# Optimization experiments

Hardware: AMD Instinct MI355X
Metric: run time of the kernel (lower is better)

The kernel has to match this reference:

```python
import jax, jax.numpy as jnp
import numpy as np
import math

HEADS = 16
ROPE_BASE = 10000.0


def _alibi_slopes(n):
    # power-of-2 branch of ALiBiBias._get_slopes (n=16 is a power of 2)
    start = 2.0 ** (-(2.0 ** (-(math.log2(n) - 3))))
    return np.array([start * (start ** i) for i in range(n)], dtype=np.float32)


def _rope_cos_sin(T, head_dim):
    # RotaryPositionalEmbedding: inv_freq over even indices, emb = cat(freqs, freqs)
    inv_freq = 1.0 / (ROPE_BASE ** (jnp.arange(0, head_dim, 2, dtype=jnp.float32) / head_dim))
    t = jnp.arange(T, dtype=jnp.float32)
    f = t[:, None] * inv_freq[None, :]            # (T, head_dim//2)
    emb = jnp.concatenate([f, f], axis=-1)        # (T, head_dim)
    # apply_rotary_pos_emb takes cos/sin of emb then strides [0::2]
    cos = jnp.cos(emb)[:, 0::2]                   # (T, head_dim//2)
    sin = jnp.sin(emb)[:, 0::2]
    return cos, sin


def _apply_rope(x, cos, sin):
    # x: (B,H,T,hd); cos/sin: (T, hd//2)
    x1 = x[..., 0::2]
    x2 = x[..., 1::2]
    r1 = x1 * cos - x2 * sin
    r2 = x2 * cos + x1 * sin
    # interleave back: out[...,0::2]=r1, out[...,1::2]=r2
    return jnp.stack([r1, r2], axis=-1).reshape(x.shape)


def setup_inputs() -> dict:
    key = jax.random.key(0)
    k1, k2, k3, k4 = jax.random.split(key, 4)
    B, T, C = 2, 2048, 1024
    x = jax.random.normal(k1, (B, T, C), dtype=jnp.float32)
    W_qkv = jax.random.normal(k2, (C, 3 * C), dtype=jnp.float32) * 0.02
    W_out = jax.random.normal(k3, (C, C), dtype=jnp.float32) * 0.02
    b_out = jax.random.normal(k4, (C,), dtype=jnp.float32) * 0.02
    return {"x": x, "W_qkv": W_qkv, "W_out": W_out, "b_out": b_out}


def reference(x, W_qkv, W_out, b_out):
    B, T, C = x.shape
    H = HEADS
    hd = C // H

    qkv = (x @ W_qkv).reshape(B, T, 3, H, hd)
    qkv = jnp.transpose(qkv, (2, 0, 3, 1, 4))     # (3, B, H, T, hd)
    q, k, v = qkv[0], qkv[1], qkv[2]

    cos, sin = _rope_cos_sin(T, hd)
    q = _apply_rope(q, cos, sin)
    k = _apply_rope(k, cos, sin)

    scores = jnp.einsum('bhqd,bhkd->bhqk', q, k) / jnp.sqrt(jnp.float32(hd))

    # ALiBi bias: -slope_h * |i - j|
    slopes = jnp.asarray(_alibi_slopes(H))        # (H,)
    pos = jnp.arange(T, dtype=jnp.float32)
    dist = jnp.abs(pos[None, :] - pos[:, None])   # (T, T)
    scores = scores - slopes[None, :, None, None] * dist[None, None, :, :]

    attn = jax.nn.softmax(scores, axis=-1)
    out = jnp.einsum('bhqk,bhkd->bhqd', attn, v)  # (B,H,T,hd)
    out = jnp.transpose(out, (0, 2, 1, 3)).reshape(B, T, C)
    out = out @ W_out + b_out
    return out, attn
```

## Files before the change

### kernel.cpp

```cpp
#include <hip/hip_runtime.h>
#include <hip/hip_bf16.h>

typedef __bf16 bf16_t;
typedef __bf16 bf16x8 __attribute__((ext_vector_type(8)));
typedef float floatx4 __attribute__((ext_vector_type(4)));

#define NB 2
#define NT 2048
#define NC 1024
#define NH 16
#define HD 64
#define BT (NB*NT)

__global__ void k_cvt_x(const float* __restrict__ x, bf16_t* __restrict__ xb, int n){
  int i = (blockIdx.x*blockDim.x + threadIdx.x)*4;
  if (i >= n) return;
  float4 v = *(const float4*)(x+i);
  bf16_t o[4] = {(bf16_t)v.x,(bf16_t)v.y,(bf16_t)v.z,(bf16_t)v.w};
  *(uint2*)(xb+i) = *(const uint2*)o;
}

__global__ void k_cvt_t(const float* __restrict__ in, bf16_t* __restrict__ out, int K, int N){
  __shared__ float tile[32][33];
  int tid = threadIdx.x;
  int kt = blockIdx.y*32, nt = blockIdx.x*32;
  int row = tid>>3, c4 = (tid&7)*4;
  float4 v = *(const float4*)(in + (size_t)(kt+row)*N + nt + c4);
  tile[row][c4+0]=v.x; tile[row][c4+1]=v.y; tile[row][c4+2]=v.z; tile[row][c4+3]=v.w;
  __syncthreads();
  bf16_t o[4];
  #pragma unroll
  for (int i=0;i<4;i++) o[i] = (bf16_t)tile[c4+i][row];
  *(uint2*)(out + (size_t)(nt+row)*K + kt + c4) = *(const uint2*)o;
}

template<bool BIAS, bool OUTBF>
__global__ __launch_bounds__(256) void k_gemm(
    const bf16_t* __restrict__ A, const bf16_t* __restrict__ Bt,
    void* __restrict__ Cv, const float* __restrict__ bias, int M, int N, int K){
  __shared__ __align__(16) bf16_t As[64][32];
  __shared__ __align__(16) bf16_t Bs[128][32];
  int tid = threadIdx.x;
  int wave = tid>>6, lane = tid&63, quad = lane>>4, l15 = lane&15;
  int m0 = blockIdx.y*64, n0 = blockIdx.x*128;
  int wm = (wave>>1)*32, wn = (wave&1)*64;
  floatx4 acc[2][4];
  #pragma unroll
  for(int i=0;i<2;i++)
    #pragma unroll
    for(int j=0;j<4;j++) acc[i][j] = (floatx4){0.f,0.f,0.f,0.f};
  int arow = tid>>2, ac8 = (tid&3)*8;
  const bf16_t* Ag  = A  + (size_t)(m0+arow)*K + ac8;
  const bf16_t* Bg0 = Bt + (size_t)(n0+arow)*K + ac8;
  const bf16_t* Bg1 = Bt + (size_t)(n0+arow+64)*K + ac8;
  for (int k0=0;k0<K;k0+=32){
    *(bf16x8*)&As[arow][ac8]    = *(const bf16x8*)(Ag  + k0);
    *(bf16x8*)&Bs[arow][ac8]    = *(const bf16x8*)(Bg0 + k0);
    *(bf16x8*)&Bs[arow+64][ac8] = *(const bf16x8*)(Bg1 + k0);
    __syncthreads();
    bf16x8 af[2], bfr[4];
    #pragma unroll
    for(int mi=0;mi<2;mi++) af[mi]  = *(const bf16x8*)&As[wm+mi*16+l15][quad*8];
    #pragma unroll
    for(int ni=0;ni<4;ni++) bfr[ni] = *(const bf16x8*)&Bs[wn+ni*16+l15][quad*8];
    #pragma unroll
    for(int mi=0;mi<2;mi++)
      #pragma unroll
      for(int ni=0;ni<4;ni++)
        acc[mi][ni] = __builtin_amdgcn_mfma_f32_16x16x32_bf16(af[mi], bfr[ni], acc[mi][ni],0,0,0);
    __syncthreads();
  }
  #pragma unroll
  for(int ni=0;ni<4;ni++){
    int col = n0 + wn + ni*16 + l15;
    float bv = 0.f; if (BIAS) bv = bias[col];
    #pragma unroll
    for(int mi=0;mi<2;mi++){
      int rowb = m0 + wm + mi*16 + quad*4;
      #pragma unroll
      for(int r=0;r<4;r++){
        float v = acc[mi][ni][r] + bv;
        if (OUTBF) ((bf16_t*)Cv)[(size_t)(rowb+r)*N + col] = (bf16_t)v;
        else       ((float*)Cv)[(size_t)(rowb+r)*N + col]  = v;
      }
    }
  }
}

__global__ void k_rope(const bf16_t* __restrict__ qkv, bf16_t* __restrict__ Qb,
                       bf16_t* __restrict__ Kb, bf16_t* __restrict__ Vb){
  int p = blockIdx.x*blockDim.x + threadIdx.x;
  int r = p / 1536;
  int c = (p - r*1536)*2;
  int s = c >> 10, rem = c & 1023;
  int h = rem >> 6, d = rem & 63, j = d >> 1;
  int b = r >> 11, t = r & 2047;
  float x1 = (float)qkv[(size_t)r*3072 + c];
  float x2 = (float)qkv[(size_t)r*3072 + c + 1];
  float o1, o2;
  if (s < 2){
    float freq = exp2f(-0.8304820237218406f * (float)(j & 15));
    float ang = (float)t * freq;
    float sn, cs;
    sincosf(ang, &sn, &cs);
    o1 = x1*cs - x2*sn;
    o2 = x2*cs + x1*sn;
  } else { o1 = x1; o2 = x2; }
  bf16_t* dst = (s==0) ? Qb : (s==1 ? Kb : Vb);
  bf16_t o[2] = {(bf16_t)o1, (bf16_t)o2};
  *(unsigned int*)(dst + (size_t)((b*NH + h)*NT + t)*HD + d) = *(const unsigned int*)o;
}

__global__ __launch_bounds__(256) void k_attn(
    const bf16_t* __restrict__ Qb, const bf16_t* __restrict__ Kb, const bf16_t* __restrict__ Vb,
    float* __restrict__ attn, bf16_t* __restrict__ Ob){
  __shared__ __align__(16) bf16_t Ks[32][72];
  __shared__ __align__(16) bf16_t Vt[64][40];
  __shared__ __align__(16) bf16_t Ps[4][16][40];
  int tid = threadIdx.x;
  int wave = tid>>6, lane = tid&63, quad = lane>>4, l15 = lane&15;
  int qt = blockIdx.x, bh = blockIdx.y;
  int h = bh & (NH-1);
  float slope = exp2f(-0.5f*(float)(h+1));
  int qbase = qt*64 + wave*16;
  const bf16_t* qrow = Qb + ((size_t)bh*NT + qbase + l15)*HD;
  bf16x8 qa0 = *(const bf16x8*)(qrow + quad*8);
  bf16x8 qa1 = *(const bf16x8*)(qrow + 32 + quad*8);
  int sr = tid>>3, sc8 = (tid&7)*8;
  const bf16_t* kbase = Kb + ((size_t)bh*NT + sr)*HD + sc8;
  const bf16_t* vbase = Vb + ((size_t)bh*NT + sr)*HD + sc8;
  const floatx4 z4 = {0.f,0.f,0.f,0.f};

  float lsum[4] = {0.f,0.f,0.f,0.f};
  for (int k0=0;k0<NT;k0+=32){
    *(bf16x8*)&Ks[sr][sc8] = *(const bf16x8*)(kbase + (size_t)k0*HD);
    __syncthreads();
    #pragma unroll
    for (int nt=0;nt<2;nt++){
      bf16x8 kb0 = *(const bf16x8*)&Ks[nt*16+l15][quad*8];
      bf16x8 kb1 = *(const bf16x8*)&Ks[nt*16+l15][32+quad*8];
      floatx4 sv = __builtin_amdgcn_mfma_f32_16x16x32_bf16(qa0, kb0, z4,0,0,0);
      sv = __builtin_amdgcn_mfma_f32_16x16x32_bf16(qa1, kb1, sv,0,0,0);
      int kpos = k0 + nt*16 + l15;
      #pragma unroll
      for (int r=0;r<4;r++){
        int qpos = qbase + quad*4 + r;
        float sc = sv[r]*0.125f - slope*fabsf((float)(qpos - kpos));
        lsum[r] += __expf(sc);
      }
    }
    __syncthreads();
  }
  #pragma unroll
  for (int r=0;r<4;r++){
    #pragma unroll
    for (int off=1;off<16;off<<=1) lsum[r] += __shfl_xor(lsum[r], off, 16);
  }
  float invl[4];
  #pragma unroll
  for (int r=0;r<4;r++) invl[r] = 1.f / lsum[r];

  floatx4 oacc[4] = {z4,z4,z4,z4};
  float* attnrow = attn + (size_t)bh*NT*NT;
  for (int k0=0;k0<NT;k0+=32){
    *(bf16x8*)&Ks[sr][sc8] = *(const bf16x8*)(kbase + (size_t)k0*HD);
    bf16x8 vl = *(const bf16x8*)(vbase + (size_t)k0*HD);
    #pragma unroll
    for (int i=0;i<8;i++) Vt[sc8+i][sr] = vl[i];
    __syncthreads();
    #pragma unroll
    for (int nt=0;nt<2;nt++){
      bf16x8 kb0 = *(const bf16x8*)&Ks[nt*16+l15][quad*8];
      bf16x8 kb1 = *(const bf16x8*)&Ks[nt*16+l15][32+quad*8];
      floatx4 sv = __builtin_amdgcn_mfma_f32_16x16x32_bf16(qa0, kb0, z4,0,0,0);
      sv = __builtin_amdgcn_mfma_f32_16x16x32_bf16(qa1, kb1, sv,0,0,0);
      int kpos = k0 + nt*16 + l15;
      #pragma unroll
      for (int r=0;r<4;r++){
        int qpos = qbase + quad*4 + r;
        float sc = sv[r]*0.125f - slope*fabsf((float)(qpos - kpos));
        float pv = __expf(sc) * invl[r];
        attnrow[(size_t)qpos*NT + kpos] = pv;
        Ps[wave][quad*4+r][nt*16+l15] = (bf16_t)pv;
      }
    }
    __syncthreads();
    bf16x8 pa = *(const bf16x8*)&Ps[wave][l15][quad*8];
    #pragma unroll
    for (int dt=0;dt<4;dt++){
      bf16x8 vb = *(const bf16x8*)&Vt[dt*16+l15][quad*8];
      oacc[dt] = __builtin_amdgcn_mfma_f32_16x16x32_bf16(pa, vb, oacc[dt],0,0,0);
    }
    __syncthreads();
  }
  int b = bh >> 4;
  #pragma unroll
  for (int dt=0;dt<4;dt++){
    #pragma unroll
    for (int r=0;r<4;r++){
      int t = qbase + quad*4 + r;
      Ob[(size_t)(b*NT + t)*NC + h*HD + dt*16 + l15] = (bf16_t)oacc[dt][r];
    }
  }
}

extern "C" void kernel_launch(void* const* d_in, const int* in_sizes, int n_in,
                              void* d_out, int out_size, void* d_ws, size_t ws_size,
                              hipStream_t stream){
  const float* x    = (const float*)d_in[0];
  const float* Wqkv = (const float*)d_in[1];
  const float* Wout = (const float*)d_in[2];
  const float* bout = (const float*)d_in[3];
  (void)in_sizes; (void)n_in; (void)out_size; (void)ws_size;

  char* ws = (char*)d_ws;
  size_t off = 0;
  auto alloc = [&](size_t elems)->bf16_t* {
    bf16_t* p = (bf16_t*)(ws + off);
    off += ((elems*sizeof(bf16_t) + 255)/256)*256;
    return p;
  };
  bf16_t* Xb   = alloc((size_t)BT*NC);
  bf16_t* Wqt  = alloc((size_t)3*NC*NC);
  bf16_t* Wot  = alloc((size_t)NC*NC);
  bf16_t* QKVb = alloc((size_t)BT*3*NC);
  bf16_t* Qb   = alloc((size_t)NB*NH*NT*HD);
  bf16_t* Kb   = alloc((size_t)NB*NH*NT*HD);
  bf16_t* Vb   = alloc((size_t)NB*NH*NT*HD);
  bf16_t* Ob   = alloc((size_t)BT*NC);

  k_cvt_x<<<(BT*NC/4)/256, 256, 0, stream>>>(x, Xb, BT*NC);
  k_cvt_t<<<dim3(3*NC/32, NC/32), 256, 0, stream>>>(Wqkv, Wqt, NC, 3*NC);
  k_cvt_t<<<dim3(NC/32,   NC/32), 256, 0, stream>>>(Wout, Wot, NC, NC);
  k_gemm<false,true><<<dim3(3*NC/128, BT/64), 256, 0, stream>>>(Xb, Wqt, (void*)QKVb, nullptr, BT, 3*NC, NC);
  k_rope<<<(BT*1536)/256, 256, 0, stream>>>(QKVb, Qb, Kb, Vb);
  float* attn = (float*)d_out + (size_t)BT*NC;
  k_attn<<<dim3(NT/64, NB*NH), 256, 0, stream>>>(Qb, Kb, Vb, attn, Ob);
  k_gemm<true,false><<<dim3(NC/128, BT/64), 256, 0, stream>>>(Ob, Wot, d_out, bout, BT, NC, NC);
}
```

Measured before the change: 812.0 us.

## Use LDS direct loads in GEMM, pre-transpose V, drop LDS staging in attention

```diff
diff --git a/kernel.cpp b/kernel.cpp
--- a/kernel.cpp
+++ b/kernel.cpp
@@ -11,6 +11,13 @@
 #define NH 16
 #define HD 64
 #define BT (NB*NT)
+
+#define ASCALE 0.1803368801111204f
+
+__device__ __forceinline__ void gload16(const bf16_t* g, bf16_t* l){
+  __builtin_amdgcn_global_load_lds((const __attribute__((address_space(1))) void*)g,
+                                   (__attribute__((address_space(3))) void*)l, 16, 0, 0);
+}
 
 __global__ void k_cvt_x(const float* __restrict__ x, bf16_t* __restrict__ xb, int n){
   int i = (blockIdx.x*blockDim.x + threadIdx.x)*4;
@@ -38,33 +45,39 @@
 __global__ __launch_bounds__(256) void k_gemm(
     const bf16_t* __restrict__ A, const bf16_t* __restrict__ Bt,
     void* __restrict__ Cv, const float* __restrict__ bias, int M, int N, int K){
-  __shared__ __align__(16) bf16_t As[64][32];
-  __shared__ __align__(16) bf16_t Bs[128][32];
+  __shared__ __align__(16) bf16_t As[128*32];
+  __shared__ __align__(16) bf16_t Bs[128*32];
   int tid = threadIdx.x;
   int wave = tid>>6, lane = tid&63, quad = lane>>4, l15 = lane&15;
-  int m0 = blockIdx.y*64, n0 = blockIdx.x*128;
-  int wm = (wave>>1)*32, wn = (wave&1)*64;
-  floatx4 acc[2][4];
-  #pragma unroll
-  for(int i=0;i<2;i++)
+  int m0 = blockIdx.y*128, n0 = blockIdx.x*128;
+  int wm = (wave>>1)*64, wn = (wave&1)*64;
+  floatx4 acc[4][4];
+  #pragma unroll
+  for(int i=0;i<4;i++)
     #pragma unroll
     for(int j=0;j<4;j++) acc[i][j] = (floatx4){0.f,0.f,0.f,0.f};
-  int arow = tid>>2, ac8 = (tid&3)*8;
-  const bf16_t* Ag  = A  + (size_t)(m0+arow)*K + ac8;
-  const bf16_t* Bg0 = Bt + (size_t)(n0+arow)*K + ac8;
-  const bf16_t* Bg1 = Bt + (size_t)(n0+arow+64)*K + ac8;
+  int r0 = tid>>2, ch8 = (tid&3)*8;
+  const bf16_t* Ag0 = A  + (size_t)(m0+r0)*K    + ch8;
+  const bf16_t* Ag1 = A  + (size_t)(m0+r0+64)*K + ch8;
+  const bf16_t* Bg0 = Bt + (size_t)(n0+r0)*K    + ch8;
+  const bf16_t* Bg1 = Bt + (size_t)(n0+r0+64)*K + ch8;
+  bf16_t* Al0 = As + (size_t)tid*8;
+  bf16_t* Al1 = As + (size_t)(256+tid)*8;
+  bf16_t* Bl0 = Bs + (size_t)tid*8;
+  bf16_t* Bl1 = Bs + (size_t)(256+tid)*8;
   for (int k0=0;k0<K;k0+=32){
-    *(bf16x8*)&As[arow][ac8]    = *(const bf16x8*)(Ag  + k0);
-    *(bf16x8*)&Bs[arow][ac8]    = *(const bf16x8*)(Bg0 + k0);
-    *(bf16x8*)&Bs[arow+64][ac8] = *(const bf16x8*)(Bg1 + k0);
+    gload16(Ag0+k0, Al0);
+    gload16(Ag1+k0, Al1);
+    gload16(Bg0+k0, Bl0);
+    gload16(Bg1+k0, Bl1);
     __syncthreads();
-    bf16x8 af[2], bfr[4];
-    #pragma unroll
-    for(int mi=0;mi<2;mi++) af[mi]  = *(const bf16x8*)&As[wm+mi*16+l15][quad*8];
-    #pragma unroll
-    for(int ni=0;ni<4;ni++) bfr[ni] = *(const bf16x8*)&Bs[wn+ni*16+l15][quad*8];
-    #pragma unroll
-    for(int mi=0;mi<2;mi++)
+    bf16x8 af[4], bfr[4];
+    #pragma unroll
+    for(int mi=0;mi<4;mi++) af[mi]  = *(const bf16x8*)&As[(wm+mi*16+l15)*32 + quad*8];
+    #pragma unroll
+    for(int ni=0;ni<4;ni++) bfr[ni] = *(const bf16x8*)&Bs[(wn+ni*16+l15)*32 + quad*8];
+    #pragma unroll
+    for(int mi=0;mi<4;mi++)
       #pragma unroll
       for(int ni=0;ni<4;ni++)
         acc[mi][ni] = __builtin_amdgcn_mfma_f32_16x16x32_bf16(af[mi], bfr[ni], acc[mi][ni],0,0,0);
@@ -75,7 +88,7 @@
     int col = n0 + wn + ni*16 + l15;
     float bv = 0.f; if (BIAS) bv = bias[col];
     #pragma unroll
-    for(int mi=0;mi<2;mi++){
+    for(int mi=0;mi<4;mi++){
       int rowb = m0 + wm + mi*16 + quad*4;
       #pragma unroll
       for(int r=0;r<4;r++){
@@ -88,7 +101,7 @@
 }
 
 __global__ void k_rope(const bf16_t* __restrict__ qkv, bf16_t* __restrict__ Qb,
-                       bf16_t* __restrict__ Kb, bf16_t* __restrict__ Vb){
+                       bf16_t* __restrict__ Kb, bf16_t* __restrict__ VT){
   int p = blockIdx.x*blockDim.x + threadIdx.x;
   int r = p / 1536;
   int c = (p - r*1536)*2;
@@ -97,101 +110,91 @@
   int b = r >> 11, t = r & 2047;
   float x1 = (float)qkv[(size_t)r*3072 + c];
   float x2 = (float)qkv[(size_t)r*3072 + c + 1];
-  float o1, o2;
   if (s < 2){
     float freq = exp2f(-0.8304820237218406f * (float)(j & 15));
     float ang = (float)t * freq;
     float sn, cs;
     sincosf(ang, &sn, &cs);
-    o1 = x1*cs - x2*sn;
-    o2 = x2*cs + x1*sn;
-  } else { o1 = x1; o2 = x2; }
-  bf16_t* dst = (s==0) ? Qb : (s==1 ? Kb : Vb);
-  bf16_t o[2] = {(bf16_t)o1, (bf16_t)o2};
-  *(unsigned int*)(dst + (size_t)((b*NH + h)*NT + t)*HD + d) = *(const unsigned int*)o;
+    float o1 = x1*cs - x2*sn;
+    float o2 = x2*cs + x1*sn;
+    if (s == 0){ o1 *= ASCALE; o2 *= ASCALE; }
+    bf16_t* dst = (s==0) ? Qb : Kb;
+    bf16_t o[2] = {(bf16_t)o1, (bf16_t)o2};
+    *(unsigned int*)(dst + (size_t)((b*NH + h)*NT + t)*HD + d) = *(const unsigned int*)o;
+  } else {
+    size_t base = ((size_t)(b*NH + h)*HD + d)*NT + t;
+    VT[base]      = (bf16_t)x1;
+    VT[base + NT] = (bf16_t)x2;
+  }
 }
 
 __global__ __launch_bounds__(256) void k_attn(
-    const bf16_t* __restrict__ Qb, const bf16_t* __restrict__ Kb, const bf16_t* __restrict__ Vb,
+    const bf16_t* __restrict__ Qb, const bf16_t* __restrict__ Kb, const bf16_t* __restrict__ VT,
     float* __restrict__ attn, bf16_t* __restrict__ Ob){
-  __shared__ __align__(16) bf16_t Ks[32][72];
-  __shared__ __align__(16) bf16_t Vt[64][40];
   __shared__ __align__(16) bf16_t Ps[4][16][40];
   int tid = threadIdx.x;
   int wave = tid>>6, lane = tid&63, quad = lane>>4, l15 = lane&15;
-  int qt = blockIdx.x, bh = blockIdx.y;
+  int bh = blockIdx.x, qt = blockIdx.y;
   int h = bh & (NH-1);
-  float slope = exp2f(-0.5f*(float)(h+1));
+  float slopeL = 1.44269504f * exp2f(-0.5f*(float)(h+1));
   int qbase = qt*64 + wave*16;
   const bf16_t* qrow = Qb + ((size_t)bh*NT + qbase + l15)*HD;
   bf16x8 qa0 = *(const bf16x8*)(qrow + quad*8);
   bf16x8 qa1 = *(const bf16x8*)(qrow + 32 + quad*8);
-  int sr = tid>>3, sc8 = (tid&7)*8;
-  const bf16_t* kbase = Kb + ((size_t)bh*NT + sr)*HD + sc8;
-  const bf16_t* vbase = Vb + ((size_t)bh*NT + sr)*HD + sc8;
+  const bf16_t* kb_base = Kb + ((size_t)bh*NT + l15)*HD + quad*8;
+  const bf16_t* vt_base = VT + ((size_t)bh*HD + l15)*NT + quad*8;
   const floatx4 z4 = {0.f,0.f,0.f,0.f};
+  float qf[4];
+  #pragma unroll
+  for (int r=0;r<4;r++) qf[r] = (float)(qbase + quad*4 + r);
 
   float lsum[4] = {0.f,0.f,0.f,0.f};
+  #pragma unroll 4
+  for (int k16=0;k16<NT;k16+=16){
+    bf16x8 kb0 = *(const bf16x8*)(kb_base + (size_t)k16*HD);
+    bf16x8 kb1 = *(const bf16x8*)(kb_base + (size_t)k16*HD + 32);
+    floatx4 sv = __builtin_amdgcn_mfma_f32_16x16x32_bf16(qa0, kb0, z4,0,0,0);
+    sv = __builtin_amdgcn_mfma_f32_16x16x32_bf16(qa1, kb1, sv,0,0,0);
+    float kf = (float)(k16 + l15);
+    #pragma unroll
+    for (int r=0;r<4;r++)
+      lsum[r] += exp2f(__builtin_fmaf(-slopeL, fabsf(qf[r]-kf), sv[r]));
+  }
+  #pragma unroll
+  for (int r=0;r<4;r++){
+    #pragma unroll
+    for (int off=1;off<16;off<<=1) lsum[r] += __shfl_xor(lsum[r], off, 16);
+  }
+  float invl[4];
+  #pragma unroll
+  for (int r=0;r<4;r++) invl[r] = 1.f / lsum[r];
+
+  floatx4 oacc[4] = {z4,z4,z4,z4};
+  float* attnrow = attn + (size_t)bh*NT*NT;
+  #pragma unroll 2
   for (int k0=0;k0<NT;k0+=32){
-    *(bf16x8*)&Ks[sr][sc8] = *(const bf16x8*)(kbase + (size_t)k0*HD);
-    __syncthreads();
     #pragma unroll
     for (int nt=0;nt<2;nt++){
-      bf16x8 kb0 = *(const bf16x8*)&Ks[nt*16+l15][quad*8];
-      bf16x8 kb1 = *(const bf16x8*)&Ks[nt*16+l15][32+quad*8];
+      int k16 = k0 + nt*16;
+      bf16x8 kb0 = *(const bf16x8*)(kb_base + (size_t)k16*HD);
+      bf16x8 kb1 = *(const bf16x8*)(kb_base + (size_t)k16*HD + 32);
       floatx4 sv = __builtin_amdgcn_mfma_f32_16x16x32_bf16(qa0, kb0, z4,0,0,0);
       sv = __builtin_amdgcn_mfma_f32_16x16x32_bf16(qa1, kb1, sv,0,0,0);
-      int kpos = k0 + nt*16 + l15;
+      float kf = (float)(k16 + l15);
+      int kpos = k16 + l15;
       #pragma unroll
       for (int r=0;r<4;r++){
-        int qpos = qbase + quad*4 + r;
-        float sc = sv[r]*0.125f - slope*fabsf((float)(qpos - kpos));
-        lsum[r] += __expf(sc);
-      }
-    }
-    __syncthreads();
-  }
-  #pragma unroll
-  for (int r=0;r<4;r++){
-    #pragma unroll
-    for (int off=1;off<16;off<<=1) lsum[r] += __shfl_xor(lsum[r], off, 16);
-  }
-  float invl[4];
-  #pragma unroll
-  for (int r=0;r<4;r++) invl[r] = 1.f / lsum[r];
-
-  floatx4 oacc[4] = {z4,z4,z4,z4};
-  float* attnrow = attn + (size_t)bh*NT*NT;
-  for (int k0=0;k0<NT;k0+=32){
-    *(bf16x8*)&Ks[sr][sc8] = *(const bf16x8*)(kbase + (size_t)k0*HD);
-    bf16x8 vl = *(const bf16x8*)(vbase + (size_t)k0*HD);
-    #pragma unroll
-    for (int i=0;i<8;i++) Vt[sc8+i][sr] = vl[i];
-    __syncthreads();
-    #pragma unroll
-    for (int nt=0;nt<2;nt++){
-      bf16x8 kb0 = *(const bf16x8*)&Ks[nt*16+l15][quad*8];
-      bf16x8 kb1 = *(const bf16x8*)&Ks[nt*16+l15][32+quad*8];
-      floatx4 sv = __builtin_amdgcn_mfma_f32_16x16x32_bf16(qa0, kb0, z4,0,0,0);
-      sv = __builtin_amdgcn_mfma_f32_16x16x32_bf16(qa1, kb1, sv,0,0,0);
-      int kpos = k0 + nt*16 + l15;
-      #pragma unroll
-      for (int r=0;r<4;r++){
-        int qpos = qbase + quad*4 + r;
-        float sc = sv[r]*0.125f - slope*fabsf((float)(qpos - kpos));
-        float pv = __expf(sc) * invl[r];
-        attnrow[(size_t)qpos*NT + kpos] = pv;
+        float pv = exp2f(__builtin_fmaf(-slopeL, fabsf(qf[r]-kf), sv[r])) * invl[r];
+        attnrow[(size_t)(qbase + quad*4 + r)*NT + kpos] = pv;
         Ps[wave][quad*4+r][nt*16+l15] = (bf16_t)pv;
       }
     }
-    __syncthreads();
     bf16x8 pa = *(const bf16x8*)&Ps[wave][l15][quad*8];
     #pragma unroll
     for (int dt=0;dt<4;dt++){
-      bf16x8 vb = *(const bf16x8*)&Vt[dt*16+l15][quad*8];
+      bf16x8 vb = *(const bf16x8*)(vt_base + (size_t)dt*16*NT + k0);
       oacc[dt] = __builtin_amdgcn_mfma_f32_16x16x32_bf16(pa, vb, oacc[dt],0,0,0);
     }
-    __syncthreads();
   }
   int b = bh >> 4;
   #pragma unroll
@@ -226,15 +229,15 @@
   bf16_t* QKVb = alloc((size_t)BT*3*NC);
   bf16_t* Qb   = alloc((size_t)NB*NH*NT*HD);
   bf16_t* Kb   = alloc((size_t)NB*NH*NT*HD);
-  bf16_t* Vb   = alloc((size_t)NB*NH*NT*HD);
+  bf16_t* VT   = alloc((size_t)NB*NH*HD*NT);
   bf16_t* Ob   = alloc((size_t)BT*NC);
 
   k_cvt_x<<<(BT*NC/4)/256, 256, 0, stream>>>(x, Xb, BT*NC);
   k_cvt_t<<<dim3(3*NC/32, NC/32), 256, 0, stream>>>(Wqkv, Wqt, NC, 3*NC);
   k_cvt_t<<<dim3(NC/32,   NC/32), 256, 0, stream>>>(Wout, Wot, NC, NC);
-  k_gemm<false,true><<<dim3(3*NC/128, BT/64), 256, 0, stream>>>(Xb, Wqt, (void*)QKVb, nullptr, BT, 3*NC, NC);
-  k_rope<<<(BT*1536)/256, 256, 0, stream>>>(QKVb, Qb, Kb, Vb);
+  k_gemm<false,true><<<dim3(3*NC/128, BT/128), 256, 0, stream>>>(Xb, Wqt, (void*)QKVb, nullptr, BT, 3*NC, NC);
+  k_rope<<<(BT*1536)/256, 256, 0, stream>>>(QKVb, Qb, Kb, VT);
   float* attn = (float*)d_out + (size_t)BT*NC;
-  k_attn<<<dim3(NT/64, NB*NH), 256, 0, stream>>>(Qb, Kb, Vb, attn, Ob);
-  k_gemm<true,false><<<dim3(NC/128, BT/64), 256, 0, stream>>>(Ob, Wot, d_out, bout, BT, NC, NC);
-}
+  k_attn<<<dim3(NB*NH, NT/64), 256, 0, stream>>>(Qb, Kb, VT, attn, Ob);
+  k_gemm<true,false><<<dim3(NC/128, BT/128), 256, 0, stream>>>(Ob, Wot, d_out, bout, BT, NC, NC);
+}
```

New measurement: 999.0 us. +23.0%, slower.
